# Kernel optimization log

Hardware: AMD Instinct MI355X
Metric: run time of the kernel (lower is better)

Reference implementation:

```python
import jax, jax.numpy as jnp
import numpy as np

# FlowNetC correlation config (matches init_kwargs)
PAD = 20           # pad_size
MAX_DISP = 20      # max_displacement
STRIDE2 = 2        # displacement stride
K = 1              # kernel_size (1x1 patch)
# stride1 = 1, corr_multiply = 1 (multiply mode)

GRID_RAD = MAX_DISP // STRIDE2           # 10
N_DISP = (2 * GRID_RAD + 1) ** 2         # 441 output channels


def _disp_offsets():
    # slice start offsets into the padded input2 for each displacement
    # (dy, dx) in {-GRID_RAD..GRID_RAD} * STRIDE2; start = PAD + d (pad == max_disp)
    d = np.arange(-GRID_RAD, GRID_RAD + 1) * STRIDE2
    dy, dx = np.meshgrid(d, d, indexing='ij')  # row-major: dy outer, dx inner
    return np.stack([PAD + dy.ravel(), PAD + dx.ravel()], axis=1).astype(np.int32)  # [441,2]


def setup_inputs() -> dict:
    key = jax.random.key(0)
    k1, k2 = jax.random.split(key)
    B, C, H, W = 8, 256, 64, 64
    input1 = jax.random.normal(k1, (B, C, H, W), dtype=jnp.float32)
    input2 = jax.random.normal(k2, (B, C, H, W), dtype=jnp.float32)
    return {"input1": input1, "input2": input2}


def reference(input1, input2):
    B, C, H, W = input1.shape
    sumelems = float(K * K * C)  # normalization used by the CUDA kernel
    # zero-pad input2 spatially by PAD (pad_size == max_displacement)
    x2p = jnp.pad(input2, ((0, 0), (0, 0), (PAD, PAD), (PAD, PAD)))
    offs = jnp.asarray(_disp_offsets())  # [441, 2] int32

    def step(carry, off):
        # window of input2 displaced by (dy, dx) relative to input1
        sl = jax.lax.dynamic_slice(x2p, (0, 0, off[0], off[1]), (B, C, H, W))
        corr = jnp.sum(input1 * sl, axis=1) / sumelems  # [B, H, W]
        return carry, corr

    _, out = jax.lax.scan(step, None, offs)       # [441, B, H, W]
    return jnp.transpose(out, (1, 0, 2, 3))       # [B, 441, H, W]
```

## Files before the change

kernel.cpp:

```cpp
#include <hip/hip_runtime.h>
#include <hip/hip_bf16.h>


typedef short    bf16x8 __attribute__((ext_vector_type(8)));
typedef float    f32x4  __attribute__((ext_vector_type(4)));
typedef unsigned u32x2  __attribute__((ext_vector_type(2)));

constexpr int CSTRIDE = 64 * 64;
constexpr int BSTRIDE = 256 * CSTRIDE;
constexpr int NCOLS   = 112;
constexpr int CSTR    = 134;

union BF2 { __hip_bfloat162 h; unsigned u; };

__device__ inline unsigned pack_bf2(float lo, float hi) {
    BF2 cv;
    cv.h = __float22bfloat162_rn(make_float2(lo, hi));
    return cv.u;
}

__global__ __launch_bounds__(512, 4)
void corr_mfma(const float* __restrict__ in1,
               const float* __restrict__ in2,
               float* __restrict__ out)
{
    __shared__ __align__(16) unsigned blds[NCOLS * CSTR];
    __shared__ float slds[21 * 65];

    const int tid  = threadIdx.x;
    const int lane = tid & 63;
    const int w    = tid >> 6;
    const int b    = blockIdx.x & 7;
    const int y    = blockIdx.x >> 3;

    const int cl = lane & 15;
    const int q  = lane >> 4;
    const int m  = w & 3;
    const int nh = w >> 2;

    const float* i1b = in1 + b * BSTRIDE;
    const float* i2b = in2 + b * BSTRIDE;

    bf16x8 afrag[8];
#pragma unroll
    for (int k = 0; k < 8; ++k) {
        const float* p = i1b + (32 * k + 8 * q) * CSTRIDE + y * 64 + 16 * m + cl;
        float v[8];
#pragma unroll
        for (int j = 0; j < 8; ++j) v[j] = p[j * CSTRIDE];
#pragma unroll
        for (int j = 0; j < 4; ++j)
            ((unsigned*)&afrag[k])[j] = pack_bf2(v[2 * j], v[2 * j + 1]);
    }

    for (int i = tid; i < 48 * 128; i += 512) {
        const int colz = i >> 7;
        const int col  = (colz < 20) ? colz : colz + 64;
        blds[col * CSTR + (i & 127)] = 0u;
    }

    const int xs  = 16 * m + cl;
    const int cd0 = q + 4 * nh;

    for (int r = 0; r < 21; ++r) {
        const int yy = y + 2 * r - 20;
        const int ob = (b * 441 + r * 21) * CSTRIDE + y * 64;

        if (yy < 0 || yy > 63) {
            for (int i = tid; i < 21 * 64; i += 512)
                out[ob + (i >> 6) * CSTRIDE + (i & 63)] = 0.f;
            continue;
        }

        {
            const float* p   = i2b + yy * 64 + xs;
            unsigned*    dst = &blds[(xs + 20) * CSTR + cd0];
#pragma unroll
            for (int i = 0; i < 16; ++i) {
                const int c  = 2 * (cd0 + 8 * i);
                const float a0 = p[c * CSTRIDE];
                const float a1 = p[(c + 1) * CSTRIDE];
                dst[8 * i] = pack_bf2(a0, a1);
            }
        }
        __syncthreads();

#pragma unroll
        for (int nn = 0; nn < 2; ++nn) {
            const int n     = m + 2 * nh + nn;
            const int baddr = (16 * n + cl) * CSTR + 4 * q;
            f32x4 acc = {0.f, 0.f, 0.f, 0.f};
#pragma unroll
            for (int k = 0; k < 8; ++k) {
                bf16x8 bfrag;
                ((u32x2*)&bfrag)[0] = *(const u32x2*)&blds[baddr + 16 * k];
                ((u32x2*)&bfrag)[1] = *(const u32x2*)&blds[baddr + 16 * k + 2];
                acc = __builtin_amdgcn_mfma_f32_16x16x32_bf16(afrag[k], bfrag, acc, 0, 0, 0);
            }
            const int gcol = 16 * n + cl;
#pragma unroll
            for (int i = 0; i < 4; ++i) {
                const int gx = 16 * m + 4 * q + i;
                const int d2 = gcol - gx;
                if (d2 >= 0 && d2 <= 40 && !(d2 & 1))
                    slds[(d2 >> 1) * 65 + gx] = acc[i];
            }
        }
        __syncthreads();

        for (int i = tid; i < 21 * 64; i += 512) {
            const int dx = i >> 6, gx = i & 63;
            out[ob + dx * CSTRIDE + gx] = slds[dx * 65 + gx] * (1.f / 256.f);
        }
    }
}

extern "C" void kernel_launch(void* const* d_in, const int* in_sizes, int n_in,
                              void* d_out, int out_size, void* d_ws, size_t ws_size,
                              hipStream_t stream) {
    const float* in1 = (const float*)d_in[0];
    const float* in2 = (const float*)d_in[1];
    float* out = (float*)d_out;
    corr_mfma<<<dim3(512), dim3(512), 0, stream>>>(in1, in2, out);
}
```

Baseline: 153.9 us.

## Pre-transpose input2 to bf16 channel-last layout in a separate kernel

Adds a prepass kernel that converts input2 to bf16 and transposes it to [B,H,W,C] in the workspace. The correlation kernel then loads each needed row with 16-byte vector loads instead of many strided fp32 loads plus per-element conversion, which it previously redid for each of the 64 output rows. The cost is an extra kernel launch, an extra pass over input2 and workspace traffic, plus an added barrier at the end of each displacement-row iteration.

```diff
diff --git a/kernel.cpp b/kernel.cpp
--- a/kernel.cpp
+++ b/kernel.cpp
@@ -12,6 +12,7 @@
 constexpr int CSTR    = 134;
 
 union BF2 { __hip_bfloat162 h; unsigned u; };
+union BF1 { __hip_bfloat16 h; unsigned short u; };
 
 __device__ inline unsigned pack_bf2(float lo, float hi) {
     BF2 cv;
@@ -19,9 +20,40 @@
     return cv.u;
 }
 
+__global__ __launch_bounds__(256)
+void conv_in2(const float* __restrict__ in2, unsigned short* __restrict__ in2t)
+{
+    __shared__ unsigned short lt[64 * 66];
+    const int tid = threadIdx.x;
+    const int b = blockIdx.x & 7;
+    const int y = blockIdx.x >> 3;
+    const float* src = in2 + b * BSTRIDE + y * 64;
+    unsigned* odw = reinterpret_cast<unsigned*>(in2t + (b * 64 + y) * (64 * 256));
+
+    for (int c0 = 0; c0 < 256; c0 += 64) {
+        __syncthreads();
+#pragma unroll
+        for (int it = 0; it < 16; ++it) {
+            const int c = it * 4 + (tid >> 6);
+            const int x = tid & 63;
+            BF1 cv; cv.h = __float2bfloat16(src[(c0 + c) * CSTRIDE + x]);
+            lt[x * 66 + c] = cv.u;
+        }
+        __syncthreads();
+        const unsigned* ldw = reinterpret_cast<const unsigned*>(lt);
+#pragma unroll
+        for (int it = 0; it < 8; ++it) {
+            const int flat = tid + 256 * it;
+            const int x  = flat >> 5;
+            const int cp = flat & 31;
+            odw[x * 128 + (c0 >> 1) + cp] = ldw[x * 33 + cp];
+        }
+    }
+}
+
 __global__ __launch_bounds__(512, 4)
 void corr_mfma(const float* __restrict__ in1,
-               const float* __restrict__ in2,
+               const unsigned short* __restrict__ in2t,
                float* __restrict__ out)
 {
     __shared__ __align__(16) unsigned blds[NCOLS * CSTR];
@@ -39,7 +71,6 @@
     const int nh = w >> 2;
 
     const float* i1b = in1 + b * BSTRIDE;
-    const float* i2b = in2 + b * BSTRIDE;
 
     bf16x8 afrag[8];
 #pragma unroll
@@ -59,9 +90,6 @@
         blds[col * CSTR + (i & 127)] = 0u;
     }
 
-    const int xs  = 16 * m + cl;
-    const int cd0 = q + 4 * nh;
-
     for (int r = 0; r < 21; ++r) {
         const int yy = y + 2 * r - 20;
         const int ob = (b * 441 + r * 21) * CSTRIDE + y * 64;
@@ -73,14 +101,17 @@
         }
 
         {
-            const float* p   = i2b + yy * 64 + xs;
-            unsigned*    dst = &blds[(xs + 20) * CSTR + cd0];
+            const uint4* src = reinterpret_cast<const uint4*>(
+                in2t + (b * 64 + yy) * (64 * 256));
 #pragma unroll
-            for (int i = 0; i < 16; ++i) {
-                const int c  = 2 * (cd0 + 8 * i);
-                const float a0 = p[c * CSTRIDE];
-                const float a1 = p[(c + 1) * CSTRIDE];
-                dst[8 * i] = pack_bf2(a0, a1);
+            for (int j = 0; j < 4; ++j) {
+                const int seg = tid + 512 * j;
+                const int x   = seg >> 5;
+                const int cw  = (seg & 31) << 2;
+                const uint4 v = src[seg];
+                unsigned* d = &blds[(x + 20) * CSTR + cw];
+                *reinterpret_cast<u32x2*>(d)     = u32x2{v.x, v.y};
+                *reinterpret_cast<u32x2*>(d + 2) = u32x2{v.z, v.w};
             }
         }
         __syncthreads();
@@ -112,6 +143,7 @@
             const int dx = i >> 6, gx = i & 63;
             out[ob + dx * CSTRIDE + gx] = slds[dx * 65 + gx] * (1.f / 256.f);
         }
+        __syncthreads();
     }
 }
 
@@ -121,5 +153,8 @@
     const float* in1 = (const float*)d_in[0];
     const float* in2 = (const float*)d_in[1];
     float* out = (float*)d_out;
-    corr_mfma<<<dim3(512), dim3(512), 0, stream>>>(in1, in2, out);
+    unsigned short* in2t = (unsigned short*)d_ws;
+
+    conv_in2<<<dim3(512), dim3(256), 0, stream>>>(in2, in2t);
+    corr_mfma<<<dim3(512), dim3(512), 0, stream>>>(in1, in2t, out);
 }
```

Measured after the change: 154.6 us. About the same (+0.5%).
